# Optimization experiments

Measured on AMD Instinct MI355X. Metric: run time of the kernel, lower is better.

## Reference

```python
import jax, jax.numpy as jnp
import numpy as np

MS = (1, 2, 4, 8, 16, 32)  # ms_token_size; last entry == H == W
A = -0.75  # PyTorch bicubic coefficient


def _cubic_w(t, a=A):
    t = abs(float(t))
    if t <= 1.0:
        return (a + 2.0) * t**3 - (a + 3.0) * t**2 + 1.0
    if t < 2.0:
        return a * t**3 - 5.0 * a * t**2 + 8.0 * a * t - 4.0 * a
    return 0.0


def _bicubic_matrix(n_in, n_out):
    # Dense [n_out, n_in] matrix reproducing F.interpolate(mode='bicubic',
    # align_corners=False) with border-clamped taps (PyTorch semantics).
    M = np.zeros((n_out, n_in), np.float32)
    s = n_in / n_out
    for i in range(n_out):
        x = (i + 0.5) * s - 0.5
        x0 = int(np.floor(x))
        t = x - x0
        for off in (-1, 0, 1, 2):
            j = min(max(x0 + off, 0), n_in - 1)
            M[i, j] += _cubic_w(off - t)
    return jnp.asarray(M)


def _area_down(x, pn):
    # 'area' interpolation with integer factor == average pooling
    B, C, H, W = x.shape
    f = H // pn
    return x.reshape(B, C, pn, f, pn, f).mean(axis=(3, 5))


def _bicubic_up(x, Mh, Mw):
    # separable bicubic: y = Mh @ x @ Mw^T per (b, c)
    return jnp.einsum('hi,wj,bcij->bchw', Mh, Mw, x)


def setup_inputs() -> dict:
    key = jax.random.key(0)
    k1, k2 = jax.random.split(key)
    z_enc = jax.random.normal(k1, (16, 128, 32, 32), dtype=jnp.float32)
    emb = jax.random.normal(k2, (8192, 128), dtype=jnp.float32) * 1.0  # std=1.0
    return {"z_enc": z_enc, "emb": emb}


def reference(z_enc, emb):
    B, C, H, W = z_enc.shape
    n_levels = len(MS)
    # z_enc is detached in the original (z_enc.detach())
    z_rest = jax.lax.stop_gradient(z_enc)
    z_dec = jnp.zeros_like(z_rest)
    e_sq = jnp.sum(emb * emb, axis=1)  # [V]
    ret = []
    for step, pn in enumerate(MS):
        last = step == n_levels - 1
        zd = z_rest if last else _area_down(z_rest, pn)
        flat = zd.transpose(0, 2, 3, 1).reshape(-1, C)  # [B*pn*pn, C]
        # ||z||^2 + ||e||^2 - 2 z e^T
        dist = jnp.sum(flat * flat, axis=1, keepdims=True) + e_sq \
               - 2.0 * (flat @ emb.T)
        token = jnp.argmin(dist, axis=1)  # [B*pn*pn]
        zq = emb[token].reshape(B, pn, pn, C).transpose(0, 3, 1, 2)  # [B,C,pn,pn]
        if last:
            zu = zq
        else:
            Mh = _bicubic_matrix(pn, H)
            Mw = _bicubic_matrix(pn, W)
            zu = _bicubic_up(zq, Mh, Mw)
        z_dec = z_dec + zu
        z_rest = z_rest - zu
        ret.append(z_dec)
    return jnp.stack(ret)  # [n_levels, B, C, H, W]
```

## Files before the change

kernel.cpp:

```cpp
#include <hip/hip_runtime.h>
#include <hip/hip_bf16.h>

#define NCODES 8192
#define CDIM 128
#define NTOT (16*128*32*32)

typedef __attribute__((ext_vector_type(8))) short bf16x8;
typedef __attribute__((ext_vector_type(16))) float f32x16;
typedef unsigned long long u64;
typedef unsigned int u32;
typedef unsigned short ushort_t;

__device__ __forceinline__ ushort_t f2bf(float x) {
    u32 u = __float_as_uint(x);
    u32 r = (u + 0x7FFFu + ((u >> 16) & 1u)) >> 16;
    return (ushort_t)r;
}
__device__ __forceinline__ float bf2f(ushort_t h) {
    return __uint_as_float(((u32)h) << 16);
}

__device__ __forceinline__ void gload_lds16(const void* g, void* l) {
    __builtin_amdgcn_global_load_lds(
        (const __attribute__((address_space(1))) unsigned int*)g,
        (__attribute__((address_space(3))) unsigned int*)l, 16, 0, 0);
}

__global__ __launch_bounds__(256) void pack_emb_kernel(const float* __restrict__ src,
        ushort_t* __restrict__ dst, float* __restrict__ esq) {
    __shared__ float sm[32][129];
    int rb = blockIdx.x, t = threadIdx.x;
    int rl = t >> 3, d0 = (t & 7) * 16;
    const float4* s4 = (const float4*)(src + (size_t)(rb * 32 + rl) * CDIM + d0);
    #pragma unroll
    for (int j = 0; j < 4; j++) {
        float4 v = s4[j];
        sm[rl][d0 + 4*j + 0] = v.x; sm[rl][d0 + 4*j + 1] = v.y;
        sm[rl][d0 + 4*j + 2] = v.z; sm[rl][d0 + 4*j + 3] = v.w;
    }
    __syncthreads();
    {
        int r = t >> 3, g = t & 7;
        float s = 0.f;
        #pragma unroll
        for (int k = 0; k < 16; k++) { float x = sm[r][g * 16 + k]; s += x * x; }
        s += __shfl_xor(s, 1, 64);
        s += __shfl_xor(s, 2, 64);
        s += __shfl_xor(s, 4, 64);
        if (g == 0) esq[rb * 32 + r] = s;
    }
    #pragma unroll
    for (int k = 0; k < 2; k++) {
        int s = t + 256 * k;
        int c = s >> 6, l = s & 63;
        int r = l & 31, dbase = c * 16 + (l >> 5) * 8;
        bf16x8 vh, vl;
        #pragma unroll
        for (int e = 0; e < 8; e++) {
            float x = sm[r][dbase + e];
            ushort_t hh = f2bf(x);
            vh[e] = (short)hh;
            vl[e] = (short)f2bf(x - bf2f(hh));
        }
        size_t base = ((size_t)(rb * 8 + c) * 2) * 512 + (size_t)l * 8;
        *(bf16x8*)(dst + base)       = vh;
        *(bf16x8*)(dst + base + 512) = vl;
    }
}

__global__ __launch_bounds__(256) void pack_kernel(const float* __restrict__ src,
        ushort_t* __restrict__ dst, u64* __restrict__ keys, int nrows, float scale) {
    __shared__ float sm[32][129];
    int rb = blockIdx.x, t = threadIdx.x;
    if (t < 32) keys[rb * 32 + t] = ~0ull;
    int rl = t >> 3, d0 = (t & 7) * 16;
    int row = rb * 32 + rl;
    if (row > nrows - 1) row = nrows - 1;
    const float4* s4 = (const float4*)(src + (size_t)row * CDIM + d0);
    #pragma unroll
    for (int j = 0; j < 4; j++) {
        float4 v = s4[j];
        sm[rl][d0 + 4*j + 0] = v.x; sm[rl][d0 + 4*j + 1] = v.y;
        sm[rl][d0 + 4*j + 2] = v.z; sm[rl][d0 + 4*j + 3] = v.w;
    }
    __syncthreads();
    #pragma unroll
    for (int k = 0; k < 2; k++) {
        int s = t + 256 * k;
        int c = s >> 6, l = s & 63;
        int r = l & 31, dbase = c * 16 + (l >> 5) * 8;
        bf16x8 vh, vl;
        #pragma unroll
        for (int e = 0; e < 8; e++) {
            float x = sm[r][dbase + e] * scale;
            ushort_t hh = f2bf(x);
            vh[e] = (short)hh;
            vl[e] = (short)f2bf(x - bf2f(hh));
        }
        size_t base = ((size_t)(rb * 8 + c) * 2) * 512 + (size_t)l * 8;
        *(bf16x8*)(dst + base)       = vh;
        *(bf16x8*)(dst + base + 512) = vl;
    }
}

__global__ __launch_bounds__(256) void pack_l5_kernel(const float* __restrict__ src,
        ushort_t* __restrict__ dst, u64* __restrict__ keys) {
    __shared__ float sm[128][36];
    int bh = blockIdx.x;
    int b = bh >> 5, h = bh & 31;
    int t = threadIdx.x;
    if (t < 32) keys[bh * 32 + t] = ~0ull;
    int d = t >> 1, w0 = (t & 1) * 16;
    const float* sp = src + (((size_t)b * CDIM + d) * 32 + h) * 32 + w0;
    #pragma unroll
    for (int j = 0; j < 16; j++) sm[d][w0 + j] = sp[j];
    __syncthreads();
    #pragma unroll
    for (int k = 0; k < 2; k++) {
        int s = t + 256 * k;
        int c = s >> 6, l = s & 63;
        int w = l & 31, dbase = c * 16 + (l >> 5) * 8;
        bf16x8 vh, vl;
        #pragma unroll
        for (int e = 0; e < 8; e++) {
            float x = sm[dbase + e][w] * -2.0f;
            ushort_t hh = f2bf(x);
            vh[e] = (short)hh;
            vl[e] = (short)f2bf(x - bf2f(hh));
        }
        size_t base = ((size_t)(bh * 8 + c) * 2) * 512 + (size_t)l * 8;
        *(bf16x8*)(dst + base)       = vh;
        *(bf16x8*)(dst + base + 512) = vl;
    }
}

__global__ __launch_bounds__(256) void down_kernel(const float* __restrict__ src,
        float* __restrict__ zd, int lf ) {
    int f  = 1 << lf;
    int ff = f * f;
    int llpi = (2 * lf > 6) ? 6 : 2 * lf;
    int lpi  = 1 << llpi;
    int epl  = ff >> llpi;
    int t    = blockIdx.x * 256 + threadIdx.x;
    int item = t >> llpi;
    int wi   = t & (lpi - 1);
    int row = item >> 7, dim = item & 127;
    int lpn = 5 - lf;
    int b  = row >> (2 * lpn);
    int rem = row & ((1 << (2 * lpn)) - 1);
    int ph = rem >> lpn, pw = rem & ((1 << lpn) - 1);
    const float* sp = src + (((size_t)b * CDIM + dim) * 32 + (ph << lf)) * 32 + (pw << lf);
    float s = 0.f;
    for (int k = 0; k < epl; k++) {
        int flat = wi * epl + k;
        int u = flat >> lf, v = flat & (f - 1);
        s += sp[u * 32 + v];
    }
    for (int d = lpi >> 1; d; d >>= 1) s += __shfl_xor(s, d, 64);
    if (wi == 0) zd[(size_t)row * CDIM + dim] = s * (1.0f / (float)ff);
}

__global__ __launch_bounds__(512) void argmin_kernel(
        const ushort_t* __restrict__ apk, const ushort_t* __restrict__ bpk,
        const float* __restrict__ esq, u64* __restrict__ keys,
        int tiles, int cps) {
    __shared__ ushort_t lds[3][8192];
    __shared__ float es_lds[1024];

    int bid = blockIdx.x;
    int q     = bid >> 3;
    int tile  = q % tiles;
    int slice = (bid & 7) + 8 * (q / tiles);
    int code0 = slice * cps;
    int steps = cps >> 5;
    int tid = threadIdx.x, wv = tid >> 6, l = tid & 63, l31 = l & 31, lh = l >> 5;

    int rb = tile * 8 + wv;
    const ushort_t* ap = apk + (size_t)rb * 8192 + l * 8;
    bf16x8 a_h[8], a_l[8];
    #pragma unroll
    for (int c = 0; c < 8; c++) {
        a_h[c] = *(const bf16x8*)(ap + (2 * c) * 512);
        a_l[c] = *(const bf16x8*)(ap + (2 * c + 1) * 512);
    }
    float ev0 = esq[code0 + (tid & (cps - 1))];
    float ev1 = esq[code0 + ((tid + 512) & (cps - 1))];
    __builtin_amdgcn_sched_barrier(0);

    const char* bbase = (const char*)bpk + (size_t)(code0 >> 5) * 16384;
    int issue = wv * 2;
    {
        const char* g0 = bbase + (size_t)issue * 1024 + (size_t)l * 16;
        gload_lds16(g0, &lds[0][issue * 512]);
        gload_lds16(g0 + 1024, &lds[0][issue * 512 + 512]);
        if (steps > 1) {
            gload_lds16(g0 + 16384, &lds[1][issue * 512]);
            gload_lds16(g0 + 17408, &lds[1][issue * 512 + 512]);
        }
    }
    __builtin_amdgcn_sched_barrier(0);
    es_lds[tid] = ev0;
    es_lds[tid + 512] = ev1;
    asm volatile("s_waitcnt lgkmcnt(0)" ::: "memory");

    float best[16];
    int   bidx[16];
    #pragma unroll
    for (int r = 0; r < 16; r++) { best[r] = 1e38f; bidx[r] = 0; }

    int cur = 0;
    for (int t = 0; t < steps; ++t) {
        if (t + 1 < steps) asm volatile("s_waitcnt vmcnt(2)" ::: "memory");
        else               asm volatile("s_waitcnt vmcnt(0)" ::: "memory");
        __builtin_amdgcn_s_barrier();
        if (t + 2 < steps) {
            const char* g = bbase + (size_t)(t + 2) * 16384
                          + (size_t)issue * 1024 + (size_t)l * 16;
            int nxt = cur + 2; if (nxt >= 3) nxt -= 3;
            ushort_t* d = &lds[nxt][issue * 512];
            gload_lds16(g, d);
            gload_lds16(g + 1024, d + 512);
        }
        float es = es_lds[(t << 5) + l31];
        f32x16 ahh, ahl, alh;
        #pragma unroll
        for (int r = 0; r < 16; r++) { ahh[r] = es; ahl[r] = 0.f; alh[r] = 0.f; }
        const ushort_t* lp = &lds[cur][0] + l * 8;
        bf16x8 vh = *(const bf16x8*)(lp);
        bf16x8 vl = *(const bf16x8*)(lp + 512);
        __builtin_amdgcn_s_setprio(1);
        #pragma unroll
        for (int c = 0; c < 8; c++) {
            bf16x8 nvh = vh, nvl = vl;
            if (c < 7) {
                nvh = *(const bf16x8*)(lp + (2 * c + 2) * 512);
                nvl = *(const bf16x8*)(lp + (2 * c + 3) * 512);
            }
            ahh = __builtin_amdgcn_mfma_f32_32x32x16_bf16(a_h[c], vh, ahh, 0, 0, 0);
            ahl = __builtin_amdgcn_mfma_f32_32x32x16_bf16(a_h[c], vl, ahl, 0, 0, 0);
            alh = __builtin_amdgcn_mfma_f32_32x32x16_bf16(a_l[c], vh, alh, 0, 0, 0);
            vh = nvh; vl = nvl;
        }
        __builtin_amdgcn_s_setprio(0);
        int code = code0 + (t << 5) + l31;
        #pragma unroll
        for (int r = 0; r < 16; r++) {
            float s = (ahh[r] + ahl[r]) + alh[r];
            bool lt = s < best[r];
            best[r] = lt ? s : best[r];
            bidx[r] = lt ? code : bidx[r];
        }
        cur = (cur + 1 == 3) ? 0 : cur + 1;
    }

    #pragma unroll
    for (int r = 0; r < 16; r++) {
        u32 fb = __float_as_uint(best[r]);
        fb = (fb & 0x80000000u) ? ~fb : (fb | 0x80000000u);
        u64 key = ((u64)fb << 32) | (u32)bidx[r];
        #pragma unroll
        for (int d = 1; d < 32; d <<= 1) {
            u64 o = __shfl_xor(key, d, 64);
            key = (o < key) ? o : key;
        }
        if (l31 == 0) {
            int rw = tile * 256 + wv * 32 + (r & 3) + 8 * (r >> 2) + 4 * lh;
            atomicMin(&keys[rw], key);
        }
    }
}

__device__ __forceinline__ float cubicw(float t) {
    float t2 = t * t;
    if (t <= 1.0f) return (1.25f * t - 2.25f) * t2 + 1.0f;
    return -0.75f * (((t - 5.0f) * t + 8.0f) * t - 4.0f);
}

__global__ __launch_bounds__(256) void up_kernel(
        const float* __restrict__ emb,
        const u64* __restrict__ keys,
        const float* __restrict__ src,
        const float* __restrict__ prev,
        float* __restrict__ zrest,
        float* __restrict__ out,
        float* __restrict__ zd_next,
        int pn, int last, int first, int pnn) {
    __shared__ float wtab[32][4];
    __shared__ int   itab[32][4];
    __shared__ float smp[512];
    int tid = threadIdx.x;
    if (!last && tid < 128) {
        int pos = tid >> 2, tap = tid & 3;
        float s  = (float)pn * (1.0f / 32.0f);
        float x  = ((float)pos + 0.5f) * s - 0.5f;
        float x0 = floorf(x);
        float t  = x - x0;
        int   off = tap - 1;
        float w  = cubicw(fabsf((float)off - t));
        int   jj = (int)x0 + off;
        jj = min(max(jj, 0), pn - 1);
        wtab[pos][tap] = w;
        itab[pos][tap] = jj;
    }
    __syncthreads();

    int t  = blockIdx.x * 256 + tid;
    int w4 = (t & 7) << 2;
    int h  = (t >> 3) & 31;
    int c  = (t >> 8) & 127;
    int b  = t >> 15;
    size_t i = (((size_t)b * CDIM + c) * 32 + h) * 32 + w4;

    float zu[4];
    if (last) {
        int kb = (b << 10) + (h << 5) + w4;
        #pragma unroll
        for (int j = 0; j < 4; j++) {
            int tok = (int)(keys[kb + j] & 0xFFFFFFFFull);
            zu[j] = emb[(size_t)tok * CDIM + c];
        }
    } else {
        int base = b * pn * pn;
        #pragma unroll
        for (int j = 0; j < 4; j++) zu[j] = 0.f;
        #pragma unroll
        for (int u = 0; u < 4; u++) {
            float whu = wtab[h][u];
            int   ih  = itab[h][u] * pn;
            #pragma unroll
            for (int j = 0; j < 4; j++) {
                float acc = 0.f;
                #pragma unroll
                for (int v = 0; v < 4; v++) {
                    int tok = (int)(keys[base + ih + itab[w4 + j][v]] & 0xFFFFFFFFull);
                    acc += wtab[w4 + j][v] * emb[(size_t)tok * CDIM + c];
                }
                zu[j] += whu * acc;
            }
        }
    }
    float4 sv = *(const float4*)(src + i);
    float4 pv = {0.f, 0.f, 0.f, 0.f};
    if (!first) pv = *(const float4*)(prev + i);
    float4 ov, rv;
    ov.x = pv.x + zu[0]; ov.y = pv.y + zu[1]; ov.z = pv.z + zu[2]; ov.w = pv.w + zu[3];
    rv.x = sv.x - zu[0]; rv.y = sv.y - zu[1]; rv.z = sv.z - zu[2]; rv.w = sv.w - zu[3];
    *(float4*)(out + i)   = ov;
    *(float4*)(zrest + i) = rv;

    if (pnn) {
        int f = 32 / pnn;
        if (f >= 4) {
            smp[h * 8 + (w4 >> 2)] = (rv.x + rv.y) + (rv.z + rv.w);
        } else {
            smp[h * 16 + (w4 >> 1)]     = rv.x + rv.y;
            smp[h * 16 + (w4 >> 1) + 1] = rv.z + rv.w;
        }
        __syncthreads();
        int W = pnn * pnn;
        if (tid < W) {
            int lb = __builtin_ctz(pnn);
            int ph = tid >> lb, pw = tid & (pnn - 1);
            float s = 0.f;
            if (f >= 4) {
                int cg = f >> 2;
                for (int u = 0; u < f; u++)
                    for (int v = 0; v < cg; v++)
                        s += smp[(ph * f + u) * 8 + pw * cg + v];
            } else {
                s = smp[(2 * ph) * 16 + pw] + smp[(2 * ph + 1) * 16 + pw];
            }
            int b2 = blockIdx.x >> 7, c2 = blockIdx.x & 127;
            int row = (b2 * pnn + ph) * pnn + pw;
            zd_next[(size_t)row * CDIM + c2] = s * (1.0f / (float)(f * f));
        }
    }
}

extern "C" void kernel_launch(void* const* d_in, const int* in_sizes, int n_in,
                              void* d_out, int out_size, void* d_ws, size_t ws_size,
                              hipStream_t stream) {
    const float* z_enc = (const float*)d_in[0];
    const float* emb   = (const float*)d_in[1];
    float* out = (float*)d_out;
    float* ws  = (float*)d_ws;

    float*    zrest  = ws;
    float*    zd_f32 = ws + 2097152;
    ushort_t* zd_pk  = (ushort_t*)(ws + 4194304);
    ushort_t* emb_pk = (ushort_t*)(ws + 6291456);
    float*    esq    = ws + 7340032;
    u64*      keys   = (u64*)(ws + 7348224);

    pack_emb_kernel<<<NCODES / 32, 256, 0, stream>>>(emb, emb_pk, esq);
    down_kernel<<<512, 256, 0, stream>>>(z_enc, zd_f32, 5);

    const int MS_[6] = {1, 2, 4, 8, 16, 32};
    const int SL_[6] = {256, 256, 256, 64, 16, 8};
    for (int lvl = 0; lvl < 6; lvl++) {
        int pn     = MS_[lvl];
        int rows   = 16 * pn * pn;
        int tiles  = (rows + 255) / 256;
        int slices = SL_[lvl];
        int cps    = NCODES / slices;
        const float* src = lvl ? zrest : z_enc;

        if (lvl < 5) {
            pack_kernel<<<tiles * 8, 256, 0, stream>>>(zd_f32, zd_pk, keys, rows, -2.0f);
        } else {
            pack_l5_kernel<<<512, 256, 0, stream>>>(zrest, zd_pk, keys);
        }
        argmin_kernel<<<tiles * slices, 512, 0, stream>>>(
            zd_pk, emb_pk, esq, keys, tiles, cps);
        int pnn = (lvl < 4) ? MS_[lvl + 1] : 0;
        up_kernel<<<NTOT / 4 / 256, 256, 0, stream>>>(
            emb, keys, src, lvl ? (out + (size_t)(lvl - 1) * NTOT) : out,
            zrest, out + (size_t)lvl * NTOT, zd_f32,
            pn, lvl == 5 ? 1 : 0, lvl == 0 ? 1 : 0, pnn);
    }
}
```

Before: 505.5 us.

## Process 64 codes per argmin step with double buffering and fused accumulators

The argmin kernel now handles 64 codebook entries per loop step as two 32-code MFMA groups, and reuses each A fragment across both groups. The three split-bf16 products are chained into a single accumulator per group instead of three separate accumulators that are summed afterwards. The LDS pipeline drops from three stages to two, with a full vmcnt(0) wait on every step. Block-to-slice mapping is simplified and slice counts are reduced, most notably to 4 for the last level. This trades fewer loop iterations and less epilogue work for less load/compute overlap and fewer blocks in flight per level.

```diff
diff --git a/kernel.cpp b/kernel.cpp
--- a/kernel.cpp
+++ b/kernel.cpp
@@ -163,16 +163,16 @@
 __global__ __launch_bounds__(512) void argmin_kernel(
         const ushort_t* __restrict__ apk, const ushort_t* __restrict__ bpk,
         const float* __restrict__ esq, u64* __restrict__ keys,
-        int tiles, int cps) {
-    __shared__ ushort_t lds[3][8192];
-    __shared__ float es_lds[1024];
-
+        int tiles, int slices) {
+    __shared__ ushort_t lds[2][16384];
+    __shared__ float es_lds[2048];
+
+    int cps = NCODES / slices;
+    int steps = cps >> 6;
     int bid = blockIdx.x;
-    int q     = bid >> 3;
-    int tile  = q % tiles;
-    int slice = (bid & 7) + 8 * (q / tiles);
+    int tile  = bid / slices;
+    int slice = bid % slices;
     int code0 = slice * cps;
-    int steps = cps >> 5;
     int tid = threadIdx.x, wv = tid >> 6, l = tid & 63, l31 = l & 31, lh = l >> 5;
 
     int rb = tile * 8 + wv;
@@ -183,24 +183,27 @@
         a_h[c] = *(const bf16x8*)(ap + (2 * c) * 512);
         a_l[c] = *(const bf16x8*)(ap + (2 * c + 1) * 512);
     }
-    float ev0 = esq[code0 + (tid & (cps - 1))];
-    float ev1 = esq[code0 + ((tid + 512) & (cps - 1))];
+    float ev0 = 0.f, ev1 = 0.f, ev2 = 0.f, ev3 = 0.f;
+    if (tid < cps)        ev0 = esq[code0 + tid];
+    if (512  + tid < cps) ev1 = esq[code0 + 512 + tid];
+    if (1024 + tid < cps) ev2 = esq[code0 + 1024 + tid];
+    if (1536 + tid < cps) ev3 = esq[code0 + 1536 + tid];
     __builtin_amdgcn_sched_barrier(0);
 
-    const char* bbase = (const char*)bpk + (size_t)(code0 >> 5) * 16384;
-    int issue = wv * 2;
+    const char* bbase = (const char*)bpk + (size_t)(code0 >> 6) * 32768;
     {
-        const char* g0 = bbase + (size_t)issue * 1024 + (size_t)l * 16;
-        gload_lds16(g0, &lds[0][issue * 512]);
-        gload_lds16(g0 + 1024, &lds[0][issue * 512 + 512]);
-        if (steps > 1) {
-            gload_lds16(g0 + 16384, &lds[1][issue * 512]);
-            gload_lds16(g0 + 17408, &lds[1][issue * 512 + 512]);
-        }
+        const char* g0 = bbase + (size_t)wv * 4096 + (size_t)l * 16;
+        ushort_t* d0 = &lds[0][wv * 2048];
+        gload_lds16(g0,        d0);
+        gload_lds16(g0 + 1024, d0 + 512);
+        gload_lds16(g0 + 2048, d0 + 1024);
+        gload_lds16(g0 + 3072, d0 + 1536);
     }
     __builtin_amdgcn_sched_barrier(0);
-    es_lds[tid] = ev0;
-    es_lds[tid + 512] = ev1;
+    if (tid < cps)        es_lds[tid] = ev0;
+    if (512  + tid < cps) es_lds[512 + tid] = ev1;
+    if (1024 + tid < cps) es_lds[1024 + tid] = ev2;
+    if (1536 + tid < cps) es_lds[1536 + tid] = ev3;
     asm volatile("s_waitcnt lgkmcnt(0)" ::: "memory");
 
     float best[16];
@@ -208,49 +211,49 @@
     #pragma unroll
     for (int r = 0; r < 16; r++) { best[r] = 1e38f; bidx[r] = 0; }
 
-    int cur = 0;
     for (int t = 0; t < steps; ++t) {
-        if (t + 1 < steps) asm volatile("s_waitcnt vmcnt(2)" ::: "memory");
-        else               asm volatile("s_waitcnt vmcnt(0)" ::: "memory");
+        asm volatile("s_waitcnt vmcnt(0)" ::: "memory");
         __builtin_amdgcn_s_barrier();
-        if (t + 2 < steps) {
-            const char* g = bbase + (size_t)(t + 2) * 16384
-                          + (size_t)issue * 1024 + (size_t)l * 16;
-            int nxt = cur + 2; if (nxt >= 3) nxt -= 3;
-            ushort_t* d = &lds[nxt][issue * 512];
-            gload_lds16(g, d);
+        if (t + 1 < steps) {
+            const char* g = bbase + (size_t)(t + 1) * 32768
+                          + (size_t)wv * 4096 + (size_t)l * 16;
+            ushort_t* d = &lds[(t + 1) & 1][wv * 2048];
+            gload_lds16(g,        d);
             gload_lds16(g + 1024, d + 512);
-        }
-        float es = es_lds[(t << 5) + l31];
-        f32x16 ahh, ahl, alh;
-        #pragma unroll
-        for (int r = 0; r < 16; r++) { ahh[r] = es; ahl[r] = 0.f; alh[r] = 0.f; }
-        const ushort_t* lp = &lds[cur][0] + l * 8;
-        bf16x8 vh = *(const bf16x8*)(lp);
-        bf16x8 vl = *(const bf16x8*)(lp + 512);
+            gload_lds16(g + 2048, d + 1024);
+            gload_lds16(g + 3072, d + 1536);
+        }
+        float es0 = es_lds[(t << 6) + l31];
+        float es1 = es_lds[(t << 6) + 32 + l31];
+        f32x16 acc0, acc1;
+        #pragma unroll
+        for (int r = 0; r < 16; r++) { acc0[r] = es0; acc1[r] = es1; }
+        const ushort_t* lp = &lds[t & 1][0] + l * 8;
         __builtin_amdgcn_s_setprio(1);
         #pragma unroll
         for (int c = 0; c < 8; c++) {
-            bf16x8 nvh = vh, nvl = vl;
-            if (c < 7) {
-                nvh = *(const bf16x8*)(lp + (2 * c + 2) * 512);
-                nvl = *(const bf16x8*)(lp + (2 * c + 3) * 512);
-            }
-            ahh = __builtin_amdgcn_mfma_f32_32x32x16_bf16(a_h[c], vh, ahh, 0, 0, 0);
-            ahl = __builtin_amdgcn_mfma_f32_32x32x16_bf16(a_h[c], vl, ahl, 0, 0, 0);
-            alh = __builtin_amdgcn_mfma_f32_32x32x16_bf16(a_l[c], vh, alh, 0, 0, 0);
-            vh = nvh; vl = nvl;
+            bf16x8 g0h = *(const bf16x8*)(lp + (2 * c) * 512);
+            bf16x8 g0l = *(const bf16x8*)(lp + (2 * c + 1) * 512);
+            bf16x8 g1h = *(const bf16x8*)(lp + 8192 + (2 * c) * 512);
+            bf16x8 g1l = *(const bf16x8*)(lp + 8192 + (2 * c + 1) * 512);
+            acc0 = __builtin_amdgcn_mfma_f32_32x32x16_bf16(a_h[c], g0h, acc0, 0, 0, 0);
+            acc1 = __builtin_amdgcn_mfma_f32_32x32x16_bf16(a_h[c], g1h, acc1, 0, 0, 0);
+            acc0 = __builtin_amdgcn_mfma_f32_32x32x16_bf16(a_h[c], g0l, acc0, 0, 0, 0);
+            acc1 = __builtin_amdgcn_mfma_f32_32x32x16_bf16(a_h[c], g1l, acc1, 0, 0, 0);
+            acc0 = __builtin_amdgcn_mfma_f32_32x32x16_bf16(a_l[c], g0h, acc0, 0, 0, 0);
+            acc1 = __builtin_amdgcn_mfma_f32_32x32x16_bf16(a_l[c], g1h, acc1, 0, 0, 0);
         }
         __builtin_amdgcn_s_setprio(0);
-        int code = code0 + (t << 5) + l31;
+        int code = code0 + (t << 6) + l31;
         #pragma unroll
         for (int r = 0; r < 16; r++) {
-            float s = (ahh[r] + ahl[r]) + alh[r];
-            bool lt = s < best[r];
-            best[r] = lt ? s : best[r];
-            bidx[r] = lt ? code : bidx[r];
-        }
-        cur = (cur + 1 == 3) ? 0 : cur + 1;
+            float s0 = acc0[r], s1 = acc1[r];
+            float m  = fminf(s0, s1);
+            int   ci = (s0 <= s1) ? code : code + 32;
+            bool lt = m < best[r];
+            best[r] = lt ? m : best[r];
+            bidx[r] = lt ? ci : bidx[r];
+        }
     }
 
     #pragma unroll
@@ -396,13 +399,12 @@
     down_kernel<<<512, 256, 0, stream>>>(z_enc, zd_f32, 5);
 
     const int MS_[6] = {1, 2, 4, 8, 16, 32};
-    const int SL_[6] = {256, 256, 256, 64, 16, 8};
+    const int SL_[6] = {128, 128, 128, 64, 16, 4};
     for (int lvl = 0; lvl < 6; lvl++) {
         int pn     = MS_[lvl];
         int rows   = 16 * pn * pn;
         int tiles  = (rows + 255) / 256;
         int slices = SL_[lvl];
-        int cps    = NCODES / slices;
         const float* src = lvl ? zrest : z_enc;
 
         if (lvl < 5) {
@@ -411,7 +413,7 @@
             pack_l5_kernel<<<512, 256, 0, stream>>>(zrest, zd_pk, keys);
         }
         argmin_kernel<<<tiles * slices, 512, 0, stream>>>(
-            zd_pk, emb_pk, esq, keys, tiles, cps);
+            zd_pk, emb_pk, esq, keys, tiles, slices);
         int pnn = (lvl < 4) ? MS_[lvl + 1] : 0;
         up_kernel<<<NTOT / 4 / 256, 256, 0, stream>>>(
             emb, keys, src, lvl ? (out + (size_t)(lvl - 1) * NTOT) : out,
```

Result: faster. 436.5 us (-13.7%).
